# Performance work log

Hardware: AMD Instinct MI355X
Metric: run time of the kernel (lower is better)

## Reference

```python
import jax, jax.numpy as jnp
import numpy as np

N = 50000      # nodes
E = 400000     # edges
HID = 128      # hidden_size
L = 3          # num_att_layer
K = 9          # rbf_size
H = 4          # heads
C = HID // H   # out_channels per head (32)
G = 512        # graphs in batch
CUTOFF = 10.0


def _rbf(D):
    # ExponentialRBF: softplus(softplus_inverse(x)) == x, so centers/widths are the raw values
    centers = jnp.linspace(1.0, float(np.exp(-CUTOFF)), K)          # (K,)
    width = (0.5 / ((1.0 - np.exp(-CUTOFF)) / K)) ** 2              # scalar
    x = D / CUTOFF
    x3 = x ** 3
    x4 = x3 * x
    x5 = x4 * x
    cut = jnp.where(x < 1.0, 1.0 - 6.0 * x5 + 15.0 * x4 - 10.0 * x3, 0.0)
    return cut[:, None] * jnp.exp(-width * (jnp.exp(-D)[:, None] - centers) ** 2)  # (E,K)


def _ln(x, g, b):
    mu = jnp.mean(x, axis=-1, keepdims=True)
    var = jnp.var(x, axis=-1, keepdims=True)
    return (x - mu) / jnp.sqrt(var + 1e-5) * g + b


def _seg_softmax(logits, seg, n):
    # numerically stable softmax over edges grouped by target node
    m = jax.ops.segment_max(logits, seg, num_segments=n)
    e = jnp.exp(logits - m[seg])
    s = jax.ops.segment_sum(e, seg, num_segments=n)
    return e / s[seg]


def setup_inputs() -> dict:
    key = jax.random.key(0)
    ks = jax.random.split(key, 32)
    s = 1.0 / np.sqrt(HID)
    se = 1.0 / np.sqrt(K + 1)
    sb = 1.0 / np.sqrt(3 * HID)
    nrm = jax.random.normal
    inp = {
        "h": nrm(ks[0], (N, HID), jnp.float32),
        "pos": nrm(ks[1], (N, 3), jnp.float32) * 3.0,
        "edge_weight": jax.random.uniform(ks[2], (E,), jnp.float32),
        "Wq": nrm(ks[3], (L, HID, HID)) * s,   "bq": nrm(ks[4], (L, HID)) * 0.01,
        "Wk": nrm(ks[5], (L, HID, HID)) * s,   "bk": nrm(ks[6], (L, HID)) * 0.01,
        "Wv": nrm(ks[7], (L, HID, HID)) * s,   "bv": nrm(ks[8], (L, HID)) * 0.01,
        "We": nrm(ks[9], (L, K + 1, HID)) * se,
        "Wskip": nrm(ks[10], (L, HID, HID)) * s, "bskip": nrm(ks[11], (L, HID)) * 0.01,
        "Wbeta": nrm(ks[12], (L, 3 * HID, 1)) * sb,
        "Wffn1": nrm(ks[13], (L, HID, HID)) * s, "bffn1": nrm(ks[14], (L, HID)) * 0.01,
        "Wffn2": nrm(ks[15], (L, HID, HID)) * s, "bffn2": nrm(ks[16], (L, HID)) * 0.01,
        "Wffn3": nrm(ks[17], (L, HID, HID)) * s, "bffn3": nrm(ks[18], (L, HID)) * 0.01,
        "ln_g": jnp.ones((HID,), jnp.float32),
        "ln_b": jnp.zeros((HID,), jnp.float32),
        "Wo1": nrm(ks[19], (HID, HID)) * s, "bo1": nrm(ks[20], (HID,)) * 0.01,
        "Wo2": nrm(ks[21], (HID, 1)) * s,   "bo2": nrm(ks[22], (1,)) * 0.01,
        "edge_index": jax.random.randint(ks[23], (2, E), 0, N),
        "batch": jnp.sort(jax.random.randint(ks[24], (N,), 0, G)),
    }
    return inp


def reference(h, pos, edge_weight, Wq, bq, Wk, bk, Wv, bv, We, Wskip, bskip, Wbeta,
              Wffn1, bffn1, Wffn2, bffn2, Wffn3, bffn3, ln_g, ln_b, Wo1, bo1, Wo2, bo2,
              edge_index, batch):
    sp = jax.nn.softplus
    n = h.shape[0]
    src, dst = edge_index[0], edge_index[1]  # source j -> target i
    D = jnp.linalg.norm(pos[dst] - pos[src], axis=-1)              # (E,)
    efeat = jnp.concatenate([_rbf(D), edge_weight[:, None]], -1)   # (E, K+1)
    inv_sqrt_c = 1.0 / np.sqrt(C)

    for i in range(L):
        hn = _ln(h, ln_g, ln_b)
        q = (hn @ Wq[i] + bq[i]).reshape(n, H, C)
        k = (hn @ Wk[i] + bk[i]).reshape(n, H, C)
        v = (hn @ Wv[i] + bv[i]).reshape(n, H, C)
        ea = (efeat @ We[i]).reshape(-1, H, C)                     # (E,H,C)
        kj = k[src] + ea
        alpha = jnp.einsum('ehc,ehc->eh', q[dst], kj) * inv_sqrt_c  # (E,H)
        alpha = _seg_softmax(alpha, dst, n)
        # dropout p=0.5 is a no-op in eval mode
        msg = (v[src] + ea) * alpha[:, :, None]
        out = jax.ops.segment_sum(msg, dst, num_segments=n).reshape(n, H * C)
        x_r = hn @ Wskip[i] + bskip[i]
        beta = jax.nn.sigmoid(jnp.concatenate([out, x_r, out - x_r], -1) @ Wbeta[i])
        out = beta * x_r + (1.0 - beta) * out
        h = hn + sp(out)
        hn2 = _ln(h, ln_g, ln_b)
        f = sp(hn2 @ Wffn1[i] + bffn1[i])
        f = sp(f @ Wffn2[i] + bffn2[i])
        f = sp(f @ Wffn3[i] + bffn3[i])
        h = hn2 + f

    pooled = jax.ops.segment_sum(h, batch, num_segments=G)          # (G, HID)
    return sp(pooled @ Wo1 + bo1) @ Wo2 + bo2                       # (G, 1)
```

## Files before the change

kernel.cpp:

```cpp
#include <hip/hip_runtime.h>
#include <hip/hip_bf16.h>
#include <math.h>

#define HID 128
#define KRBF 9
#define NLAYER 3
#define IPAD 136

typedef __attribute__((ext_vector_type(8))) short bf16x8;
typedef __attribute__((ext_vector_type(4))) float f32x4;

__device__ __forceinline__ float sp_(float x){ return fmaxf(x,0.f) + log1pf(expf(-fabsf(x))); }
__device__ __forceinline__ float sigm_(float x){ return 1.f/(1.f+expf(-x)); }
__device__ __forceinline__ float b2f(short s){
  union{unsigned u; float f;} x; x.u = ((unsigned)(unsigned short)s)<<16; return x.f;
}
__device__ __forceinline__ short f2bs(float x){
  __hip_bfloat16 b = __float2bfloat16(x);
  return *reinterpret_cast<short*>(&b);
}
__device__ __forceinline__ float wsum64(float v){
  #pragma unroll
  for(int m=1;m<64;m<<=1) v += __shfl_xor(v,m,64);
  return v;
}
__device__ __forceinline__ float wsum16(float v){
  #pragma unroll
  for(int m=1;m<16;m<<=1) v += __shfl_xor(v,m,64);
  return v;
}
__device__ __forceinline__ float2 ldbf2(const __hip_bfloat16* p){
  __hip_bfloat162 b = *(const __hip_bfloat162*)p;
  return make_float2(__bfloat162float(b.x), __bfloat162float(b.y));
}
__device__ __forceinline__ int lb_(const int* __restrict__ a, int n, int key){
  int lo=0, hi=n;
  while(lo<hi){ int mid=(lo+hi)>>1; if(a[mid]<key) lo=mid+1; else hi=mid; }
  return lo;
}

__global__ void count_dst(const int* __restrict__ ei, int* __restrict__ counts, int E){
  int e = blockIdx.x*256+threadIdx.x;
  if(e<E) atomicAdd(&counts[ei[E+e]],1);
}
__global__ void scan1(const int* __restrict__ counts, int* __restrict__ tmp,
                      int* __restrict__ bsums, int N){
  __shared__ int lds[256];
  int t = threadIdx.x; int idx = blockIdx.x*256+t;
  int v = (idx<N)? counts[idx]:0;
  lds[t]=v; __syncthreads();
  for(int off=1;off<256;off<<=1){
    int x = (t>=off)? lds[t-off]:0;
    __syncthreads();
    lds[t]+=x; __syncthreads();
  }
  if(idx<N) tmp[idx]=lds[t];
  if(t==255) bsums[blockIdx.x]=lds[255];
}
__global__ void scan2(const int* __restrict__ bsums, int* __restrict__ boffs, int nb){
  __shared__ int lds[256];
  int t=threadIdx.x;
  int v = (t<nb)? bsums[t]:0;
  lds[t]=v; __syncthreads();
  for(int off=1;off<256;off<<=1){
    int x=(t>=off)?lds[t-off]:0;
    __syncthreads();
    lds[t]+=x; __syncthreads();
  }
  if(t<nb) boffs[t] = lds[t]-v;
}
__global__ void finalize_rs(const int* __restrict__ tmp, const int* __restrict__ boffs,
                            int* __restrict__ row_start, int N){
  int idx = blockIdx.x*256+threadIdx.x;
  if(idx<N) row_start[idx+1] = tmp[idx] + boffs[idx>>8];
  if(idx==0) row_start[0]=0;
}
__global__ void csr_scatter(const int* __restrict__ ei, const int* __restrict__ rowst,
                            int* __restrict__ counts2, int* __restrict__ csr, int E){
  int e = blockIdx.x*256+threadIdx.x;
  if(e>=E) return;
  int d = ei[E+e];
  int p = rowst[d] + atomicAdd(&counts2[d],1);
  csr[p] = e;
}
__global__ void sort_seg(const int* __restrict__ rowst, int* __restrict__ csr, int N){
  int n = blockIdx.x*256+threadIdx.x;
  if(n>=N) return;
  int lo=rowst[n], hi=rowst[n+1];
  for(int i=lo+1;i<hi;i++){
    int v=csr[i]; int j=i-1;
    while(j>=lo && csr[j]>v){ csr[j+1]=csr[j]; j--; }
    csr[j+1]=v;
  }
}
__global__ void edge_feat(const float* __restrict__ pos, const float* __restrict__ ew,
                          const int* __restrict__ ei, const int* __restrict__ csr,
                          float* __restrict__ efs, int* __restrict__ esrc, int E){
  int p = blockIdx.x*256 + threadIdx.x;
  if(p>=E) return;
  int e = csr[p];
  int s = ei[e], d = ei[E+e];
  float dx = pos[d*3+0]-pos[s*3+0];
  float dy = pos[d*3+1]-pos[s*3+1];
  float dz = pos[d*3+2]-pos[s*3+2];
  float D = sqrtf(dx*dx+dy*dy+dz*dz);
  float x = D*0.1f;
  float cut = 0.f;
  if(x < 1.f){ float x3=x*x*x, x4=x3*x, x5=x4*x; cut = 1.f - 6.f*x5 + 15.f*x4 - 10.f*x3; }
  float ed = expf(-D);
  const double e10 = 4.5399929762484854e-05;
  const float step  = (float)((e10 - 1.0)/8.0);
  const float width = (float)((4.5/(1.0-e10))*(4.5/(1.0-e10)));
  float r12[12];
  #pragma unroll
  for(int k=0;k<KRBF;k++){
    float c = 1.0f + k*step;
    float dd = ed - c;
    r12[k] = cut*expf(-width*dd*dd);
  }
  r12[9] = ew[e]; r12[10]=0.f; r12[11]=0.f;
  float* o = efs + (size_t)p*12;
  *(float4*)&o[0] = *(float4*)&r12[0];
  *(float4*)&o[4] = *(float4*)&r12[4];
  *(float4*)&o[8] = *(float4*)&r12[8];
  esrc[p] = s;
}

__global__ void pack_w(const float* __restrict__ Wq, const float* __restrict__ Wk,
                       const float* __restrict__ Wv, const float* __restrict__ Wsk,
                       const float* __restrict__ bq, const float* __restrict__ bk,
                       const float* __restrict__ bv, const float* __restrict__ bsk,
                       const float* __restrict__ We,
                       const float* __restrict__ W1, const float* __restrict__ W2,
                       const float* __restrict__ W3,
                       __hip_bfloat16* __restrict__ Wqkvs, float* __restrict__ bqkvs,
                       __hip_bfloat16* __restrict__ Wffn){
  int idx = blockIdx.x*256 + threadIdx.x;
  const int QT = NLAYER*5*16384;
  const int FT = NLAYER*3*16384;
  const int BT = NLAYER*640;
  if(idx < QT){
    int l = idx / (5*16384);
    int rem = idx - l*(5*16384);
    int cb = rem >> 14;
    int t = rem & 16383;
    int j = t&7; int lane = (t>>3)&63; int blk = t>>9;
    int kc = blk>>3, nj = blk&7, ql = lane>>4, il = lane&15;
    int k = kc*32 + ql*8 + j;
    int gcol = cb*128 + il*8 + nj;
    float v = 0.f;
    if(gcol < 512){
      const float* src = (gcol<128)?Wq:((gcol<256)?Wk:((gcol<384)?Wv:Wsk));
      v = src[(size_t)l*16384 + k*128 + (gcol&127)];
    } else if(gcol < 552){
      int jj = gcol-512; int h=jj/10; int r=jj-10*h;
      const float* wq = Wq + (size_t)l*16384 + k*128;
      const float* we = We + (size_t)l*1280 + r*128;
      float acc=0.f;
      #pragma unroll 8
      for(int c=32*h;c<32*h+32;c++) acc = fmaf(wq[c], we[c], acc);
      v = acc;
    }
    Wqkvs[idx] = __float2bfloat16(v);
  } else if(idx < QT+FT){
    int r0 = idx - QT;
    int l = r0 / (3*16384);
    int rem = r0 - l*(3*16384);
    int f = rem >> 14;
    int t = rem & 16383;
    int j = t&7; int lane = (t>>3)&63; int blk = t>>9;
    int kc = blk>>3, nj = blk&7, ql = lane>>4, il = lane&15;
    int k = kc*32 + ql*8 + j;
    int gcol = il*8 + nj;
    const float* src = (f==0)?W1:((f==1)?W2:W3);
    Wffn[r0] = __float2bfloat16(src[(size_t)l*16384 + k*128 + gcol]);
  } else if(idx < QT+FT+BT){
    int j = idx - QT - FT;
    int l = j/640; int col = j - l*640;
    float v = 0.f;
    if(col<512){
      const float* src = (col<128)?bq:((col<256)?bk:((col<384)?bv:bsk));
      v = src[l*128 + (col&127)];
    } else if(col<552){
      int jj=col-512; int h=jj/10; int r=jj-10*h;
      const float* bqp = bq + l*128;
      const float* we = We + (size_t)l*1280 + r*128;
      float acc=0.f;
      for(int c=32*h;c<32*h+32;c++) acc = fmaf(bqp[c], we[c], acc);
      v = acc;
    }
    bqkvs[j] = v;
  }
}

__global__ void ln_node(const float* __restrict__ h, const float* __restrict__ g,
                        const float* __restrict__ b, __hip_bfloat16* __restrict__ hn, int N){
  int n = blockIdx.x*4 + (threadIdx.x>>6);
  if(n>=N) return;
  int lane = threadIdx.x & 63;
  int c = 2*lane;
  float2 v = *(const float2*)&h[(size_t)n*HID + c];
  float s1 = wsum64(v.x+v.y);
  float s2 = wsum64(v.x*v.x+v.y*v.y);
  float mu = s1*(1.f/HID);
  float var = s2*(1.f/HID) - mu*mu;
  float rs = rsqrtf(var + 1e-5f);
  __hip_bfloat162 o;
  o.x = __float2bfloat16((v.x-mu)*rs*g[c]   + b[c]);
  o.y = __float2bfloat16((v.y-mu)*rs*g[c+1] + b[c+1]);
  *(__hip_bfloat162*)&hn[(size_t)n*HID + c] = o;
}

__global__ __launch_bounds__(256) void gemm_qkvs(
    const __hip_bfloat16* __restrict__ A, const __hip_bfloat16* __restrict__ Wt,
    const float* __restrict__ bias,
    __hip_bfloat16* __restrict__ qsO, __hip_bfloat16* __restrict__ kvO,
    float* __restrict__ qwO, int N){
  __shared__ __hip_bfloat16 WsF[16384];
  int row0 = blockIdx.y*128;
  int cb = blockIdx.x;
  int tid = threadIdx.x;
  {
    const __hip_bfloat16* Wp = Wt + (size_t)cb*16384;
    #pragma unroll
    for(int i=0;i<8;i++){
      int o = (tid + 256*i)*8;
      *(float4*)&WsF[o] = *(const float4*)&Wp[o];
    }
  }
  int lane = tid&63;
  int m0 = (tid>>6)*32;
  int ql = lane>>4, il = lane&15;
  bf16x8 af[2][4];
  #pragma unroll
  for(int mi=0;mi<2;mi++){
    int r = row0 + m0 + mi*16 + il;
    r = (r < N) ? r : (N-1);
    const __hip_bfloat16* ap = A + (size_t)r*128 + ql*8;
    #pragma unroll
    for(int kc=0;kc<4;kc++) af[mi][kc] = *(const bf16x8*)(ap + kc*32);
  }
  __syncthreads();
  f32x4 acc[2][8];
  #pragma unroll
  for(int mi=0;mi<2;mi++)
    #pragma unroll
    for(int nj=0;nj<8;nj++) acc[mi][nj] = (f32x4){0.f,0.f,0.f,0.f};
  #pragma unroll
  for(int kc=0;kc<4;kc++){
    #pragma unroll
    for(int nj=0;nj<8;nj++){
      bf16x8 bb = *(bf16x8*)&WsF[((kc*8+nj)*64 + lane)*8];
      #pragma unroll
      for(int mi=0;mi<2;mi++)
        acc[mi][nj] = __builtin_amdgcn_mfma_f32_16x16x32_bf16(af[mi][kc], bb, acc[mi][nj], 0,0,0);
    }
  }
  float bl8[8];
  {
    float4 b0 = *(const float4*)&bias[cb*128 + il*8];
    float4 b1 = *(const float4*)&bias[cb*128 + il*8 + 4];
    bl8[0]=b0.x; bl8[1]=b0.y; bl8[2]=b0.z; bl8[3]=b0.w;
    bl8[4]=b1.x; bl8[5]=b1.y; bl8[6]=b1.z; bl8[7]=b1.w;
  }
  #pragma unroll
  for(int mi=0;mi<2;mi++){
    #pragma unroll
    for(int r=0;r<4;r++){
      int rr = row0 + m0 + mi*16 + ql*4 + r;
      if(rr >= N) continue;
      if(cb < 4){
        bf16x8 o;
        #pragma unroll
        for(int nj=0;nj<8;nj++) o[nj] = f2bs(acc[mi][nj][r] + bl8[nj]);
        __hip_bfloat16* dst;
        if(cb==0)      dst = qsO + (size_t)rr*256 + il*8;
        else if(cb==1) dst = kvO + (size_t)rr*256 + il*8;
        else if(cb==2) dst = kvO + (size_t)rr*256 + 128 + il*8;
        else           dst = qsO + (size_t)rr*256 + 128 + il*8;
        *(bf16x8*)dst = o;
      } else if(il < 5){
        #pragma unroll
        for(int nj=0;nj<8;nj++){
          int g = il*8 + nj;
          int h = g/10, rb = g - 10*h;
          qwO[(size_t)rr*48 + h*12 + rb] = acc[mi][nj][r] + bl8[nj];
        }
      }
    }
  }
}

__global__ __launch_bounds__(256) void attn_fused6(
    const __hip_bfloat16* __restrict__ qs, const __hip_bfloat16* __restrict__ kvb,
    const float* __restrict__ qwb, const float* __restrict__ efs,
    const int* __restrict__ esrc, const float* __restrict__ WeL,
    const int* __restrict__ rowst, float* __restrict__ att, int N){
  int n = blockIdx.x*4 + (threadIdx.x>>6);
  if(n>=N) return;
  int lane = threadIdx.x & 63;
  int eg = lane>>4, sl = lane&15;
  int c8 = sl*8, hd = sl>>2;
  const __hip_bfloat16* rowq = qs + (size_t)n*256;
  float q8[8];
  {
    bf16x8 qv = *(const bf16x8*)&rowq[c8];
    #pragma unroll
    for(int j=0;j<8;j++) q8[j] = b2f(qv[j]);
  }
  const float* qwp = qwb + (size_t)n*48 + hd*12;
  float4 qa = *(const float4*)qwp;
  float4 qb = *(const float4*)(qwp+4);
  float2 qc = *(const float2*)(qwp+8);
  float QW[10] = {qa.x,qa.y,qa.z,qa.w,qb.x,qb.y,qb.z,qb.w,qc.x,qc.y};
  int lo = rowst[n], hi = rowst[n+1];
  float ssum = 0.f, a8[8], S[10];
  #pragma unroll
  for(int j=0;j<8;j++) a8[j]=0.f;
  #pragma unroll
  for(int r=0;r<10;r++) S[r]=0.f;
  for(int i=lo+eg; i<hi; i+=4){
    int s = esrc[i];
    const __hip_bfloat16* kr = kvb + (size_t)s*256;
    bf16x8 kc = *(const bf16x8*)&kr[c8];
    bf16x8 vc = *(const bf16x8*)&kr[128 + c8];
    const float* ef = efs + (size_t)i*12;
    float4 e0 = *(const float4*)&ef[0];
    float4 e1 = *(const float4*)&ef[4];
    float2 e2 = *(const float2*)&ef[8];
    float d = 0.f;
    #pragma unroll
    for(int j=0;j<8;j++) d = fmaf(q8[j], b2f(kc[j]), d);
    d += __shfl_xor(d,1,64); d += __shfl_xor(d,2,64);
    float lg = d;
    lg = fmaf(e0.x,QW[0],lg); lg = fmaf(e0.y,QW[1],lg);
    lg = fmaf(e0.z,QW[2],lg); lg = fmaf(e0.w,QW[3],lg);
    lg = fmaf(e1.x,QW[4],lg); lg = fmaf(e1.y,QW[5],lg);
    lg = fmaf(e1.z,QW[6],lg); lg = fmaf(e1.w,QW[7],lg);
    lg = fmaf(e2.x,QW[8],lg); lg = fmaf(e2.y,QW[9],lg);
    lg *= 0.17677669529663687f;
    lg = fminf(lg, 80.f);
    float w = __expf(lg);
    ssum += w;
    #pragma unroll
    for(int j=0;j<8;j++) a8[j] = fmaf(w, b2f(vc[j]), a8[j]);
    S[0]=fmaf(w,e0.x,S[0]); S[1]=fmaf(w,e0.y,S[1]); S[2]=fmaf(w,e0.z,S[2]);
    S[3]=fmaf(w,e0.w,S[3]); S[4]=fmaf(w,e1.x,S[4]); S[5]=fmaf(w,e1.y,S[5]);
    S[6]=fmaf(w,e1.z,S[6]); S[7]=fmaf(w,e1.w,S[7]); S[8]=fmaf(w,e2.x,S[8]);
    S[9]=fmaf(w,e2.y,S[9]);
  }
  float o8[8];
  #pragma unroll
  for(int j=0;j<8;j++) o8[j]=a8[j];
  #pragma unroll
  for(int r=0;r<10;r++){
    float s=S[r];
    float4 wa = *(const float4*)&WeL[r*128+c8];
    float4 wb = *(const float4*)&WeL[r*128+c8+4];
    o8[0]=fmaf(s,wa.x,o8[0]); o8[1]=fmaf(s,wa.y,o8[1]);
    o8[2]=fmaf(s,wa.z,o8[2]); o8[3]=fmaf(s,wa.w,o8[3]);
    o8[4]=fmaf(s,wb.x,o8[4]); o8[5]=fmaf(s,wb.y,o8[5]);
    o8[6]=fmaf(s,wb.z,o8[6]); o8[7]=fmaf(s,wb.w,o8[7]);
  }
  #pragma unroll
  for(int m=16;m<64;m<<=1){
    ssum += __shfl_xor(ssum,m,64);
    #pragma unroll
    for(int j=0;j<8;j++) o8[j] += __shfl_xor(o8[j],m,64);
  }
  if(eg==0){
    float inv = (hi>lo)? 1.f/ssum : 0.f;
    float4 v0 = make_float4(o8[0]*inv, o8[1]*inv, o8[2]*inv, o8[3]*inv);
    float4 v1 = make_float4(o8[4]*inv, o8[5]*inv, o8[6]*inv, o8[7]*inv);
    *(float4*)&att[(size_t)n*128 + c8]     = v0;
    *(float4*)&att[(size_t)n*128 + c8 + 4] = v1;
  }
}

__global__ void combine_ln(const float* __restrict__ att, const __hip_bfloat16* __restrict__ qs,
                           const __hip_bfloat16* __restrict__ hn, const float* __restrict__ Wb,
                           const float* __restrict__ g, const float* __restrict__ b,
                           __hip_bfloat16* __restrict__ hn2, int N){
  int n = blockIdx.x*4 + (threadIdx.x>>6);
  if(n>=N) return;
  int lane = threadIdx.x&63;
  int c = 2*lane;
  float2 o  = *(const float2*)&att[(size_t)n*HID+c];
  float2 xr = ldbf2(&qs[(size_t)n*256 + 128 + c]);
  float bl = o.x*Wb[c] + o.y*Wb[c+1]
           + xr.x*Wb[HID+c] + xr.y*Wb[HID+c+1]
           + (o.x-xr.x)*Wb[2*HID+c] + (o.y-xr.y)*Wb[2*HID+c+1];
  bl = wsum64(bl);
  float beta = sigm_(bl);
  float u0 = beta*xr.x + (1.f-beta)*o.x;
  float u1 = beta*xr.y + (1.f-beta)*o.y;
  float2 hnv = ldbf2(&hn[(size_t)n*HID+c]);
  float h0 = hnv.x + sp_(u0);
  float h1 = hnv.y + sp_(u1);
  float s1 = wsum64(h0+h1);
  float s2 = wsum64(h0*h0+h1*h1);
  float mu = s1*(1.f/HID);
  float var = s2*(1.f/HID)-mu*mu;
  float rs = rsqrtf(var+1e-5f);
  __hip_bfloat162 outv;
  outv.x = __float2bfloat16((h0-mu)*rs*g[c]+b[c]);
  outv.y = __float2bfloat16((h1-mu)*rs*g[c+1]+b[c+1]);
  *(__hip_bfloat162*)&hn2[(size_t)n*HID+c] = outv;
}

__global__ __launch_bounds__(256) void ffn_fused(
    const __hip_bfloat16* __restrict__ hn2, const __hip_bfloat16* __restrict__ Wf,
    const float* __restrict__ b1, const float* __restrict__ b2,
    const float* __restrict__ b3, const float* __restrict__ lng,
    const float* __restrict__ lnb, float* __restrict__ hout,
    __hip_bfloat16* __restrict__ hnout, int N){
  __shared__ __hip_bfloat16 WsF[16384];
  __shared__ __hip_bfloat16 inter[2][64][IPAD];
  int row0 = blockIdx.x*64;
  int tid = threadIdx.x, lane = tid&63, wv = tid>>6;
  int ql = lane>>4, il = lane&15;

  auto stage = [&](const __hip_bfloat16* Wp){
    #pragma unroll
    for(int i=0;i<8;i++){
      int o = (tid + 256*i)*8;
      *(float4*)&WsF[o] = *(const float4*)&Wp[o];
    }
  };
  auto loadbias = [&](const float* bp, float* bl8){
    float4 x0 = *(const float4*)&bp[il*8];
    float4 x1 = *(const float4*)&bp[il*8+4];
    bl8[0]=x0.x; bl8[1]=x0.y; bl8[2]=x0.z; bl8[3]=x0.w;
    bl8[4]=x1.x; bl8[5]=x1.y; bl8[6]=x1.z; bl8[7]=x1.w;
  };

  f32x4 acc[8];
  bf16x8 af[4];
  stage(Wf);
  {
    int r = row0 + wv*16 + il;
    r = (r<N)? r : (N-1);
    const __hip_bfloat16* ap = hn2 + (size_t)r*128 + ql*8;
    #pragma unroll
    for(int kc=0;kc<4;kc++) af[kc] = *(const bf16x8*)(ap + kc*32);
  }
  __syncthreads();
  #pragma unroll
  for(int nj=0;nj<8;nj++) acc[nj] = (f32x4){0.f,0.f,0.f,0.f};
  #pragma unroll
  for(int kc=0;kc<4;kc++)
    #pragma unroll
    for(int nj=0;nj<8;nj++){
      bf16x8 bb = *(bf16x8*)&WsF[((kc*8+nj)*64 + lane)*8];
      acc[nj] = __builtin_amdgcn_mfma_f32_16x16x32_bf16(af[kc], bb, acc[nj], 0,0,0);
    }
  {
    float bl8[8]; loadbias(b1, bl8);
    #pragma unroll
    for(int r=0;r<4;r++){
      int lr = wv*16 + ql*4 + r;
      bf16x8 o;
      #pragma unroll
      for(int nj=0;nj<8;nj++) o[nj] = f2bs(sp_(acc[nj][r] + bl8[nj]));
      *(bf16x8*)&inter[0][lr][il*8] = o;
    }
  }
  __syncthreads();
  stage(Wf + 16384);
  #pragma unroll
  for(int kc=0;kc<4;kc++) af[kc] = *(bf16x8*)&inter[0][wv*16+il][ql*8 + kc*32];
  __syncthreads();
  #pragma unroll
  for(int nj=0;nj<8;nj++) acc[nj] = (f32x4){0.f,0.f,0.f,0.f};
  #pragma unroll
  for(int kc=0;kc<4;kc++)
    #pragma unroll
    for(int nj=0;nj<8;nj++){
      bf16x8 bb = *(bf16x8*)&WsF[((kc*8+nj)*64 + lane)*8];
      acc[nj] = __builtin_amdgcn_mfma_f32_16x16x32_bf16(af[kc], bb, acc[nj], 0,0,0);
    }
  {
    float bl8[8]; loadbias(b2, bl8);
    #pragma unroll
    for(int r=0;r<4;r++){
      int lr = wv*16 + ql*4 + r;
      bf16x8 o;
      #pragma unroll
      for(int nj=0;nj<8;nj++) o[nj] = f2bs(sp_(acc[nj][r] + bl8[nj]));
      *(bf16x8*)&inter[1][lr][il*8] = o;
    }
  }
  __syncthreads();
  stage(Wf + 2*16384);
  #pragma unroll
  for(int kc=0;kc<4;kc++) af[kc] = *(bf16x8*)&inter[1][wv*16+il][ql*8 + kc*32];
  __syncthreads();
  #pragma unroll
  for(int nj=0;nj<8;nj++) acc[nj] = (f32x4){0.f,0.f,0.f,0.f};
  #pragma unroll
  for(int kc=0;kc<4;kc++)
    #pragma unroll
    for(int nj=0;nj<8;nj++){
      bf16x8 bb = *(bf16x8*)&WsF[((kc*8+nj)*64 + lane)*8];
      acc[nj] = __builtin_amdgcn_mfma_f32_16x16x32_bf16(af[kc], bb, acc[nj], 0,0,0);
    }
  {
    float bl8[8]; loadbias(b3, bl8);
    float lg8[8], lb8[8];
    loadbias(lng, lg8); loadbias(lnb, lb8);
    #pragma unroll
    for(int r=0;r<4;r++){
      int rr = row0 + wv*16 + ql*4 + r;
      if(rr >= N) continue;
      bf16x8 rv = *(const bf16x8*)&hn2[(size_t)rr*128 + il*8];
      float t8[8], s1=0.f, s2=0.f;
      #pragma unroll
      for(int nj=0;nj<8;nj++){
        float x = sp_(acc[nj][r] + bl8[nj]) + b2f(rv[nj]);
        t8[nj]=x; s1+=x; s2+=x*x;
      }
      s1 = wsum16(s1); s2 = wsum16(s2);
      float mu = s1*(1.f/128.f);
      float var = s2*(1.f/128.f) - mu*mu;
      float rsg = rsqrtf(var + 1e-5f);
      *(float4*)&hout[(size_t)rr*128 + il*8]     = make_float4(t8[0],t8[1],t8[2],t8[3]);
      *(float4*)&hout[(size_t)rr*128 + il*8 + 4] = make_float4(t8[4],t8[5],t8[6],t8[7]);
      bf16x8 o;
      #pragma unroll
      for(int nj=0;nj<8;nj++) o[nj] = f2bs((t8[nj]-mu)*rsg*lg8[nj] + lb8[nj]);
      *(bf16x8*)&hnout[(size_t)rr*128 + il*8] = o;
    }
  }
}

__global__ void pool_head(const float* __restrict__ h, const int* __restrict__ batch,
                          const float* __restrict__ Wo1, const float* __restrict__ bo1,
                          const float* __restrict__ Wo2, const float* __restrict__ bo2,
                          float* __restrict__ out, int N){
  int gid = blockIdx.x;
  int t = threadIdx.x;
  int lo = lb_(batch, N, gid), hi = lb_(batch, N, gid+1);
  __shared__ float pl[128];
  __shared__ float red[128];
  float s = 0.f;
  for(int i=lo;i<hi;i++) s += h[(size_t)i*HID + t];
  pl[t] = s;
  __syncthreads();
  float acc = bo1[t];
  for(int c=0;c<128;c++) acc = fmaf(pl[c], Wo1[c*HID+t], acc);
  red[t] = sp_(acc)*Wo2[t];
  __syncthreads();
  for(int off=64;off>0;off>>=1){
    if(t<off) red[t]+=red[t+off];
    __syncthreads();
  }
  if(t==0) out[gid] = red[0] + bo2[0];
}

extern "C" void kernel_launch(void* const* d_in, const int* in_sizes, int n_in,
                              void* d_out, int out_size, void* d_ws, size_t ws_size,
                              hipStream_t stream){
  const float* h_in = (const float*)d_in[0];
  const float* pos  = (const float*)d_in[1];
  const float* ew   = (const float*)d_in[2];
  const float* Wq = (const float*)d_in[3];  const float* bq = (const float*)d_in[4];
  const float* Wk = (const float*)d_in[5];  const float* bk = (const float*)d_in[6];
  const float* Wv = (const float*)d_in[7];  const float* bv = (const float*)d_in[8];
  const float* We = (const float*)d_in[9];
  const float* Wsk= (const float*)d_in[10]; const float* bsk=(const float*)d_in[11];
  const float* Wbeta=(const float*)d_in[12];
  const float* W1=(const float*)d_in[13]; const float* b1=(const float*)d_in[14];
  const float* W2=(const float*)d_in[15]; const float* b2=(const float*)d_in[16];
  const float* W3=(const float*)d_in[17]; const float* b3=(const float*)d_in[18];
  const float* lng=(const float*)d_in[19]; const float* lnb=(const float*)d_in[20];
  const float* Wo1=(const float*)d_in[21]; const float* bo1=(const float*)d_in[22];
  const float* Wo2=(const float*)d_in[23]; const float* bo2=(const float*)d_in[24];
  const int* ei    = (const int*)d_in[25];
  const int* batch = (const int*)d_in[26];
  int N = in_sizes[0]/HID;
  int E = in_sizes[2];
  int G = out_size;
  float* out = (float*)d_out;

  char* ws = (char*)d_ws;
  size_t off=0;
  auto alloc=[&](size_t bytes)->char*{
    char* p = ws + off;
    off = (off + bytes + 255) & ~(size_t)255;
    return p;
  };
  float* efs   =(float*)alloc((size_t)E*12*4);
  int* esrc    =(int*)  alloc((size_t)E*4);
  int* csr     =(int*)  alloc((size_t)E*4);
  int* counts  =(int*)  alloc((size_t)N*4);
  int* counts2 =(int*)  alloc((size_t)N*4);
  int* rowst   =(int*)  alloc((size_t)(N+1)*4);
  int* tmp     =(int*)  alloc((size_t)N*4);
  int* bsums   =(int*)  alloc(256*4);
  int* boffs   =(int*)  alloc(256*4);
  __hip_bfloat16* hn   =(__hip_bfloat16*)alloc((size_t)N*HID*2);
  __hip_bfloat16* hn2  =(__hip_bfloat16*)alloc((size_t)N*HID*2);
  __hip_bfloat16* qsb  =(__hip_bfloat16*)alloc((size_t)N*256*2);
  __hip_bfloat16* kvb  =(__hip_bfloat16*)alloc((size_t)N*256*2);
  float* qwb   =(float*)alloc((size_t)N*48*4);
  float* att   =(float*)alloc((size_t)N*HID*4);
  float* hcur  =(float*)alloc((size_t)N*HID*4);
  __hip_bfloat16* Wqkvs_t =(__hip_bfloat16*)alloc((size_t)NLAYER*5*16384*2);
  __hip_bfloat16* Wffn_t  =(__hip_bfloat16*)alloc((size_t)NLAYER*3*16384*2);
  float* bqkvs =(float*)alloc((size_t)NLAYER*640*4);
  size_t ws_used = off;

  int ebl = (E+255)/256;
  int nb  = (N+255)/256;
  int nwb = (N+3)/4;
  int nrb128 = (N+127)/128;
  int nrb64  = (N+63)/64;
  dim3 gqkvs(5, nrb128);

  hipMemsetAsync(ws, 0, (ws_used <= ws_size ? ws_used : ws_size), stream);

  count_dst<<<ebl,256,0,stream>>>(ei,counts,E);
  scan1<<<nb,256,0,stream>>>(counts,tmp,bsums,N);
  scan2<<<1,256,0,stream>>>(bsums,boffs,nb);
  finalize_rs<<<nb,256,0,stream>>>(tmp,boffs,rowst,N);
  csr_scatter<<<ebl,256,0,stream>>>(ei,rowst,counts2,csr,E);
  sort_seg<<<nb,256,0,stream>>>(rowst,csr,N);
  edge_feat<<<ebl,256,0,stream>>>(pos,ew,ei,csr,efs,esrc,E);
  {
    int tot = NLAYER*5*16384 + NLAYER*3*16384 + NLAYER*640;
    pack_w<<<(tot+255)/256,256,0,stream>>>(Wq,Wk,Wv,Wsk,bq,bk,bv,bsk,We,W1,W2,W3,
                                           Wqkvs_t,bqkvs,Wffn_t);
  }

  ln_node<<<nwb,256,0,stream>>>(h_in,lng,lnb,hn,N);
  for(int l=0;l<NLAYER;l++){
    const float* We_l = We + (size_t)l*(KRBF+1)*HID;
    const float* Wb_l = Wbeta + (size_t)l*3*HID;
    const float* b1_l = b1 + (size_t)l*HID;
    const float* b2_l = b2 + (size_t)l*HID;
    const float* b3_l = b3 + (size_t)l*HID;

    gemm_qkvs<<<gqkvs,256,0,stream>>>(hn, Wqkvs_t + (size_t)l*5*16384,
                                      bqkvs + l*640, qsb, kvb, qwb, N);
    attn_fused6<<<nwb,256,0,stream>>>(qsb,kvb,qwb,efs,esrc,We_l,rowst,att,N);
    combine_ln<<<nwb,256,0,stream>>>(att,qsb,hn,Wb_l,lng,lnb,hn2,N);
    ffn_fused<<<nrb64,256,0,stream>>>(hn2, Wffn_t + (size_t)l*3*16384,
                                      b1_l,b2_l,b3_l,lng,lnb,hcur,hn,N);
  }
  pool_head<<<G,128,0,stream>>>(hcur,batch,Wo1,bo1,Wo2,bo2,out,N);
}
```

Baseline: 883.1 us.

## Switch activations to fp32 and emulate fp32 GEMMs with split-bf16 MFMAs

Replaces bf16 activation storage with fp32 throughout (hn, q/k/v/skip, FFN intermediates). The GEMMs now split each fp32 operand into hi/mid/lo bf16 parts and issue six MFMAs per tile, with weights read straight from global memory instead of being staged in LDS. Softplus and sigmoid now use fast __expf/__logf intrinsics. The aim is accuracy close to fp32, paid for with twice the gather bandwidth in attention, six times the MFMA work, and extra weight traffic.

```diff
diff --git a/kernel.cpp b/kernel.cpp
--- a/kernel.cpp
+++ b/kernel.cpp
@@ -5,13 +5,15 @@
 #define HID 128
 #define KRBF 9
 #define NLAYER 3
-#define IPAD 136
+#define IPADF 132
 
 typedef __attribute__((ext_vector_type(8))) short bf16x8;
 typedef __attribute__((ext_vector_type(4))) float f32x4;
 
-__device__ __forceinline__ float sp_(float x){ return fmaxf(x,0.f) + log1pf(expf(-fabsf(x))); }
-__device__ __forceinline__ float sigm_(float x){ return 1.f/(1.f+expf(-x)); }
+__device__ __forceinline__ float sp_(float x){
+  return fmaxf(x,0.f) + __logf(1.f + __expf(-fabsf(x)));
+}
+__device__ __forceinline__ float sigm_(float x){ return 1.f/(1.f+__expf(-x)); }
 __device__ __forceinline__ float b2f(short s){
   union{unsigned u; float f;} x; x.u = ((unsigned)(unsigned short)s)<<16; return x.f;
 }
@@ -19,6 +21,16 @@
   __hip_bfloat16 b = __float2bfloat16(x);
   return *reinterpret_cast<short*>(&b);
 }
+__device__ __forceinline__ void split3_8(const float* a, bf16x8& hi, bf16x8& mi, bf16x8& lo){
+  #pragma unroll
+  for(int j=0;j<8;j++){
+    float x = a[j];
+    short h = f2bs(x); hi[j]=h;
+    float r1 = x - b2f(h);
+    short m = f2bs(r1); mi[j]=m;
+    lo[j] = f2bs(r1 - b2f(m));
+  }
+}
 __device__ __forceinline__ float wsum64(float v){
   #pragma unroll
   for(int m=1;m<64;m<<=1) v += __shfl_xor(v,m,64);
@@ -28,10 +40,6 @@
   #pragma unroll
   for(int m=1;m<16;m<<=1) v += __shfl_xor(v,m,64);
   return v;
-}
-__device__ __forceinline__ float2 ldbf2(const __hip_bfloat16* p){
-  __hip_bfloat162 b = *(const __hip_bfloat162*)p;
-  return make_float2(__bfloat162float(b.x), __bfloat162float(b.y));
 }
 __device__ __forceinline__ int lb_(const int* __restrict__ a, int n, int key){
   int lo=0, hi=n;
@@ -161,7 +169,13 @@
       for(int c=32*h;c<32*h+32;c++) acc = fmaf(wq[c], we[c], acc);
       v = acc;
     }
-    Wqkvs[idx] = __float2bfloat16(v);
+    short hi = f2bs(v);
+    float r1 = v - b2f(hi);
+    short mi = f2bs(r1);
+    short lo = f2bs(r1 - b2f(mi));
+    Wqkvs[idx]        = *reinterpret_cast<__hip_bfloat16*>(&hi);
+    Wqkvs[QT + idx]   = *reinterpret_cast<__hip_bfloat16*>(&mi);
+    Wqkvs[2*QT + idx] = *reinterpret_cast<__hip_bfloat16*>(&lo);
   } else if(idx < QT+FT){
     int r0 = idx - QT;
     int l = r0 / (3*16384);
@@ -173,7 +187,14 @@
     int k = kc*32 + ql*8 + j;
     int gcol = il*8 + nj;
     const float* src = (f==0)?W1:((f==1)?W2:W3);
-    Wffn[r0] = __float2bfloat16(src[(size_t)l*16384 + k*128 + gcol]);
+    float v = src[(size_t)l*16384 + k*128 + gcol];
+    short hi = f2bs(v);
+    float r1 = v - b2f(hi);
+    short mi = f2bs(r1);
+    short lo = f2bs(r1 - b2f(mi));
+    Wffn[r0]        = *reinterpret_cast<__hip_bfloat16*>(&hi);
+    Wffn[FT + r0]   = *reinterpret_cast<__hip_bfloat16*>(&mi);
+    Wffn[2*FT + r0] = *reinterpret_cast<__hip_bfloat16*>(&lo);
   } else if(idx < QT+FT+BT){
     int j = idx - QT - FT;
     int l = j/640; int col = j - l*640;
@@ -194,7 +215,7 @@
 }
 
 __global__ void ln_node(const float* __restrict__ h, const float* __restrict__ g,
-                        const float* __restrict__ b, __hip_bfloat16* __restrict__ hn, int N){
+                        const float* __restrict__ b, float* __restrict__ hn, int N){
   int n = blockIdx.x*4 + (threadIdx.x>>6);
   if(n>=N) return;
   int lane = threadIdx.x & 63;
@@ -205,55 +226,68 @@
   float mu = s1*(1.f/HID);
   float var = s2*(1.f/HID) - mu*mu;
   float rs = rsqrtf(var + 1e-5f);
-  __hip_bfloat162 o;
-  o.x = __float2bfloat16((v.x-mu)*rs*g[c]   + b[c]);
-  o.y = __float2bfloat16((v.y-mu)*rs*g[c+1] + b[c+1]);
-  *(__hip_bfloat162*)&hn[(size_t)n*HID + c] = o;
-}
+  float2 o;
+  o.x = (v.x-mu)*rs*g[c]   + b[c];
+  o.y = (v.y-mu)*rs*g[c+1] + b[c+1];
+  *(float2*)&hn[(size_t)n*HID + c] = o;
+}
+
+#define MFMA6(ACC, AH, AM, AL, BH, BM, BL)                                    \
+  ACC = __builtin_amdgcn_mfma_f32_16x16x32_bf16(AH, BH, ACC, 0,0,0);          \
+  ACC = __builtin_amdgcn_mfma_f32_16x16x32_bf16(AM, BH, ACC, 0,0,0);          \
+  ACC = __builtin_amdgcn_mfma_f32_16x16x32_bf16(AH, BM, ACC, 0,0,0);          \
+  ACC = __builtin_amdgcn_mfma_f32_16x16x32_bf16(AL, BH, ACC, 0,0,0);          \
+  ACC = __builtin_amdgcn_mfma_f32_16x16x32_bf16(AM, BM, ACC, 0,0,0);          \
+  ACC = __builtin_amdgcn_mfma_f32_16x16x32_bf16(AH, BL, ACC, 0,0,0);
 
 __global__ __launch_bounds__(256) void gemm_qkvs(
-    const __hip_bfloat16* __restrict__ A, const __hip_bfloat16* __restrict__ Wt,
+    const float* __restrict__ A, const __hip_bfloat16* __restrict__ Whi,
+    const __hip_bfloat16* __restrict__ Wmi, const __hip_bfloat16* __restrict__ Wlo,
     const float* __restrict__ bias,
-    __hip_bfloat16* __restrict__ qsO, __hip_bfloat16* __restrict__ kvO,
+    float* __restrict__ qsO, float* __restrict__ kvO,
     float* __restrict__ qwO, int N){
-  __shared__ __hip_bfloat16 WsF[16384];
   int row0 = blockIdx.y*128;
   int cb = blockIdx.x;
   int tid = threadIdx.x;
-  {
-    const __hip_bfloat16* Wp = Wt + (size_t)cb*16384;
-    #pragma unroll
-    for(int i=0;i<8;i++){
-      int o = (tid + 256*i)*8;
-      *(float4*)&WsF[o] = *(const float4*)&Wp[o];
-    }
-  }
   int lane = tid&63;
   int m0 = (tid>>6)*32;
   int ql = lane>>4, il = lane&15;
-  bf16x8 af[2][4];
-  #pragma unroll
-  for(int mi=0;mi<2;mi++){
-    int r = row0 + m0 + mi*16 + il;
+  const __hip_bfloat16* Wh = Whi + (size_t)cb*16384;
+  const __hip_bfloat16* Wm = Wmi + (size_t)cb*16384;
+  const __hip_bfloat16* Wl = Wlo + (size_t)cb*16384;
+  bf16x8 ah[2][4], am[2][4], al[2][4];
+  #pragma unroll
+  for(int mi2=0;mi2<2;mi2++){
+    int r = row0 + m0 + mi2*16 + il;
     r = (r < N) ? r : (N-1);
-    const __hip_bfloat16* ap = A + (size_t)r*128 + ql*8;
-    #pragma unroll
-    for(int kc=0;kc<4;kc++) af[mi][kc] = *(const bf16x8*)(ap + kc*32);
-  }
-  __syncthreads();
+    const float* ap = A + (size_t)r*128 + ql*8;
+    #pragma unroll
+    for(int kc=0;kc<4;kc++){
+      float a8[8];
+      float4 a0 = *(const float4*)(ap + kc*32);
+      float4 a1 = *(const float4*)(ap + kc*32 + 4);
+      a8[0]=a0.x;a8[1]=a0.y;a8[2]=a0.z;a8[3]=a0.w;
+      a8[4]=a1.x;a8[5]=a1.y;a8[6]=a1.z;a8[7]=a1.w;
+      split3_8(a8, ah[mi2][kc], am[mi2][kc], al[mi2][kc]);
+    }
+  }
   f32x4 acc[2][8];
   #pragma unroll
-  for(int mi=0;mi<2;mi++)
-    #pragma unroll
-    for(int nj=0;nj<8;nj++) acc[mi][nj] = (f32x4){0.f,0.f,0.f,0.f};
+  for(int mi2=0;mi2<2;mi2++)
+    #pragma unroll
+    for(int nj=0;nj<8;nj++) acc[mi2][nj] = (f32x4){0.f,0.f,0.f,0.f};
   #pragma unroll
   for(int kc=0;kc<4;kc++){
     #pragma unroll
     for(int nj=0;nj<8;nj++){
-      bf16x8 bb = *(bf16x8*)&WsF[((kc*8+nj)*64 + lane)*8];
+      size_t bo = (size_t)((kc*8+nj)*64 + lane)*8;
+      bf16x8 bh = *(const bf16x8*)&Wh[bo];
+      bf16x8 bm = *(const bf16x8*)&Wm[bo];
+      bf16x8 bl = *(const bf16x8*)&Wl[bo];
       #pragma unroll
-      for(int mi=0;mi<2;mi++)
-        acc[mi][nj] = __builtin_amdgcn_mfma_f32_16x16x32_bf16(af[mi][kc], bb, acc[mi][nj], 0,0,0);
+      for(int mi2=0;mi2<2;mi2++){
+        MFMA6(acc[mi2][nj], ah[mi2][kc], am[mi2][kc], al[mi2][kc], bh, bm, bl)
+      }
     }
   }
   float bl8[8];
@@ -264,35 +298,36 @@
     bl8[4]=b1.x; bl8[5]=b1.y; bl8[6]=b1.z; bl8[7]=b1.w;
   }
   #pragma unroll
-  for(int mi=0;mi<2;mi++){
+  for(int mi2=0;mi2<2;mi2++){
     #pragma unroll
     for(int r=0;r<4;r++){
-      int rr = row0 + m0 + mi*16 + ql*4 + r;
+      int rr = row0 + m0 + mi2*16 + ql*4 + r;
       if(rr >= N) continue;
       if(cb < 4){
-        bf16x8 o;
+        float o8[8];
         #pragma unroll
-        for(int nj=0;nj<8;nj++) o[nj] = f2bs(acc[mi][nj][r] + bl8[nj]);
-        __hip_bfloat16* dst;
+        for(int nj=0;nj<8;nj++) o8[nj] = acc[mi2][nj][r] + bl8[nj];
+        float* dst;
         if(cb==0)      dst = qsO + (size_t)rr*256 + il*8;
         else if(cb==1) dst = kvO + (size_t)rr*256 + il*8;
         else if(cb==2) dst = kvO + (size_t)rr*256 + 128 + il*8;
         else           dst = qsO + (size_t)rr*256 + 128 + il*8;
-        *(bf16x8*)dst = o;
+        *(float4*)dst     = make_float4(o8[0],o8[1],o8[2],o8[3]);
+        *(float4*)(dst+4) = make_float4(o8[4],o8[5],o8[6],o8[7]);
       } else if(il < 5){
         #pragma unroll
         for(int nj=0;nj<8;nj++){
           int g = il*8 + nj;
           int h = g/10, rb = g - 10*h;
-          qwO[(size_t)rr*48 + h*12 + rb] = acc[mi][nj][r] + bl8[nj];
+          qwO[(size_t)rr*48 + h*12 + rb] = acc[mi2][nj][r] + bl8[nj];
         }
       }
     }
   }
 }
 
-__global__ __launch_bounds__(256) void attn_fused6(
-    const __hip_bfloat16* __restrict__ qs, const __hip_bfloat16* __restrict__ kvb,
+__global__ __launch_bounds__(256) void attn_fused7(
+    const float* __restrict__ qs, const float* __restrict__ kvb,
     const float* __restrict__ qwb, const float* __restrict__ efs,
     const int* __restrict__ esrc, const float* __restrict__ WeL,
     const int* __restrict__ rowst, float* __restrict__ att, int N){
@@ -301,12 +336,13 @@
   int lane = threadIdx.x & 63;
   int eg = lane>>4, sl = lane&15;
   int c8 = sl*8, hd = sl>>2;
-  const __hip_bfloat16* rowq = qs + (size_t)n*256;
+  const float* rowq = qs + (size_t)n*256;
   float q8[8];
   {
-    bf16x8 qv = *(const bf16x8*)&rowq[c8];
-    #pragma unroll
-    for(int j=0;j<8;j++) q8[j] = b2f(qv[j]);
+    float4 q0 = *(const float4*)&rowq[c8];
+    float4 q1 = *(const float4*)&rowq[c8+4];
+    q8[0]=q0.x;q8[1]=q0.y;q8[2]=q0.z;q8[3]=q0.w;
+    q8[4]=q1.x;q8[5]=q1.y;q8[6]=q1.z;q8[7]=q1.w;
   }
   const float* qwp = qwb + (size_t)n*48 + hd*12;
   float4 qa = *(const float4*)qwp;
@@ -321,16 +357,17 @@
   for(int r=0;r<10;r++) S[r]=0.f;
   for(int i=lo+eg; i<hi; i+=4){
     int s = esrc[i];
-    const __hip_bfloat16* kr = kvb + (size_t)s*256;
-    bf16x8 kc = *(const bf16x8*)&kr[c8];
-    bf16x8 vc = *(const bf16x8*)&kr[128 + c8];
+    const float* kr = kvb + (size_t)s*256;
+    float4 k0 = *(const float4*)&kr[c8];
+    float4 k1 = *(const float4*)&kr[c8+4];
+    float4 v0 = *(const float4*)&kr[128+c8];
+    float4 v1 = *(const float4*)&kr[128+c8+4];
     const float* ef = efs + (size_t)i*12;
     float4 e0 = *(const float4*)&ef[0];
     float4 e1 = *(const float4*)&ef[4];
     float2 e2 = *(const float2*)&ef[8];
-    float d = 0.f;
-    #pragma unroll
-    for(int j=0;j<8;j++) d = fmaf(q8[j], b2f(kc[j]), d);
+    float d = q8[0]*k0.x + q8[1]*k0.y + q8[2]*k0.z + q8[3]*k0.w
+            + q8[4]*k1.x + q8[5]*k1.y + q8[6]*k1.z + q8[7]*k1.w;
     d += __shfl_xor(d,1,64); d += __shfl_xor(d,2,64);
     float lg = d;
     lg = fmaf(e0.x,QW[0],lg); lg = fmaf(e0.y,QW[1],lg);
@@ -342,8 +379,10 @@
     lg = fminf(lg, 80.f);
     float w = __expf(lg);
     ssum += w;
-    #pragma unroll
-    for(int j=0;j<8;j++) a8[j] = fmaf(w, b2f(vc[j]), a8[j]);
+    a8[0]=fmaf(w,v0.x,a8[0]); a8[1]=fmaf(w,v0.y,a8[1]);
+    a8[2]=fmaf(w,v0.z,a8[2]); a8[3]=fmaf(w,v0.w,a8[3]);
+    a8[4]=fmaf(w,v1.x,a8[4]); a8[5]=fmaf(w,v1.y,a8[5]);
+    a8[6]=fmaf(w,v1.z,a8[6]); a8[7]=fmaf(w,v1.w,a8[7]);
     S[0]=fmaf(w,e0.x,S[0]); S[1]=fmaf(w,e0.y,S[1]); S[2]=fmaf(w,e0.z,S[2]);
     S[3]=fmaf(w,e0.w,S[3]); S[4]=fmaf(w,e1.x,S[4]); S[5]=fmaf(w,e1.y,S[5]);
     S[6]=fmaf(w,e1.z,S[6]); S[7]=fmaf(w,e1.w,S[7]); S[8]=fmaf(w,e2.x,S[8]);
@@ -377,16 +416,16 @@
   }
 }
 
-__global__ void combine_ln(const float* __restrict__ att, const __hip_bfloat16* __restrict__ qs,
-                           const __hip_bfloat16* __restrict__ hn, const float* __restrict__ Wb,
+__global__ void combine_ln(const float* __restrict__ att, float* __restrict__ qs,
+                           const float* __restrict__ hn, const float* __restrict__ Wb,
                            const float* __restrict__ g, const float* __restrict__ b,
-                           __hip_bfloat16* __restrict__ hn2, int N){
+                           int N){
   int n = blockIdx.x*4 + (threadIdx.x>>6);
   if(n>=N) return;
   int lane = threadIdx.x&63;
   int c = 2*lane;
   float2 o  = *(const float2*)&att[(size_t)n*HID+c];
-  float2 xr = ldbf2(&qs[(size_t)n*256 + 128 + c]);
+  float2 xr = *(const float2*)&qs[(size_t)n*256 + 128 + c];
   float bl = o.x*Wb[c] + o.y*Wb[c+1]
            + xr.x*Wb[HID+c] + xr.y*Wb[HID+c+1]
            + (o.x-xr.x)*Wb[2*HID+c] + (o.y-xr.y)*Wb[2*HID+c+1];
@@ -394,7 +433,7 @@
   float beta = sigm_(bl);
   float u0 = beta*xr.x + (1.f-beta)*o.x;
   float u1 = beta*xr.y + (1.f-beta)*o.y;
-  float2 hnv = ldbf2(&hn[(size_t)n*HID+c]);
+  float2 hnv = *(const float2*)&hn[(size_t)n*HID+c];
   float h0 = hnv.x + sp_(u0);
   float h1 = hnv.y + sp_(u1);
   float s1 = wsum64(h0+h1);
@@ -402,108 +441,111 @@
   float mu = s1*(1.f/HID);
   float var = s2*(1.f/HID)-mu*mu;
   float rs = rsqrtf(var+1e-5f);
-  __hip_bfloat162 outv;
-  outv.x = __float2bfloat16((h0-mu)*rs*g[c]+b[c]);
-  outv.y = __float2bfloat16((h1-mu)*rs*g[c+1]+b[c+1]);
-  *(__hip_bfloat162*)&hn2[(size_t)n*HID+c] = outv;
+  float2 outv;
+  outv.x = (h0-mu)*rs*g[c]+b[c];
+  outv.y = (h1-mu)*rs*g[c+1]+b[c+1];
+  *(float2*)&qs[(size_t)n*256 + c] = outv;
 }
 
 __global__ __launch_bounds__(256) void ffn_fused(
-    const __hip_bfloat16* __restrict__ hn2, const __hip_bfloat16* __restrict__ Wf,
+    const float* __restrict__ hn2,
+    const __hip_bfloat16* __restrict__ Wfhi, const __hip_bfloat16* __restrict__ Wfmi,
+    const __hip_bfloat16* __restrict__ Wflo,
     const float* __restrict__ b1, const float* __restrict__ b2,
     const float* __restrict__ b3, const float* __restrict__ lng,
     const float* __restrict__ lnb, float* __restrict__ hout,
-    __hip_bfloat16* __restrict__ hnout, int N){
-  __shared__ __hip_bfloat16 WsF[16384];
-  __shared__ __hip_bfloat16 inter[2][64][IPAD];
+    float* __restrict__ hnout, int N){
+  __shared__ float inter[2][64][IPADF];
   int row0 = blockIdx.x*64;
   int tid = threadIdx.x, lane = tid&63, wv = tid>>6;
   int ql = lane>>4, il = lane&15;
 
-  auto stage = [&](const __hip_bfloat16* Wp){
-    #pragma unroll
-    for(int i=0;i<8;i++){
-      int o = (tid + 256*i)*8;
-      *(float4*)&WsF[o] = *(const float4*)&Wp[o];
-    }
-  };
   auto loadbias = [&](const float* bp, float* bl8){
     float4 x0 = *(const float4*)&bp[il*8];
     float4 x1 = *(const float4*)&bp[il*8+4];
     bl8[0]=x0.x; bl8[1]=x0.y; bl8[2]=x0.z; bl8[3]=x0.w;
     bl8[4]=x1.x; bl8[5]=x1.y; bl8[6]=x1.z; bl8[7]=x1.w;
   };
+  auto gemm_stage = [&](const __hip_bfloat16* Wh, const __hip_bfloat16* Wm,
+                        const __hip_bfloat16* Wl,
+                        bf16x8* ah, bf16x8* am, bf16x8* al, f32x4* acc){
+    #pragma unroll
+    for(int nj=0;nj<8;nj++) acc[nj] = (f32x4){0.f,0.f,0.f,0.f};
+    #pragma unroll
+    for(int kc=0;kc<4;kc++)
+      #pragma unroll
+      for(int nj=0;nj<8;nj++){
+        size_t bo = (size_t)((kc*8+nj)*64 + lane)*8;
+        bf16x8 bh = *(const bf16x8*)&Wh[bo];
+        bf16x8 bm = *(const bf16x8*)&Wm[bo];
+        bf16x8 bl = *(const bf16x8*)&Wl[bo];
+        MFMA6(acc[nj], ah[kc], am[kc], al[kc], bh, bm, bl)
+      }
+  };
 
   f32x4 acc[8];
-  bf16x8 af[4];
-  stage(Wf);
+  bf16x8 ah[4], am[4], al[4];
   {
     int r = row0 + wv*16 + il;
     r = (r<N)? r : (N-1);
-    const __hip_bfloat16* ap = hn2 + (size_t)r*128 + ql*8;
-    #pragma unroll
-    for(int kc=0;kc<4;kc++) af[kc] = *(const bf16x8*)(ap + kc*32);
-  }
-  __syncthreads();
-  #pragma unroll
-  for(int nj=0;nj<8;nj++) acc[nj] = (f32x4){0.f,0.f,0.f,0.f};
-  #pragma unroll
-  for(int kc=0;kc<4;kc++)
-    #pragma unroll
-    for(int nj=0;nj<8;nj++){
-      bf16x8 bb = *(bf16x8*)&WsF[((kc*8+nj)*64 + lane)*8];
-      acc[nj] = __builtin_amdgcn_mfma_f32_16x16x32_bf16(af[kc], bb, acc[nj], 0,0,0);
-    }
+    const float* ap = hn2 + (size_t)r*256 + ql*8;
+    #pragma unroll
+    for(int kc=0;kc<4;kc++){
+      float a8[8];
+      float4 a0 = *(const float4*)(ap + kc*32);
+      float4 a1 = *(const float4*)(ap + kc*32 + 4);
+      a8[0]=a0.x;a8[1]=a0.y;a8[2]=a0.z;a8[3]=a0.w;
+      a8[4]=a1.x;a8[5]=a1.y;a8[6]=a1.z;a8[7]=a1.w;
+      split3_8(a8, ah[kc], am[kc], al[kc]);
+    }
+  }
+  gemm_stage(Wfhi, Wfmi, Wflo, ah, am, al, acc);
   {
     float bl8[8]; loadbias(b1, bl8);
     #pragma unroll
     for(int r=0;r<4;r++){
       int lr = wv*16 + ql*4 + r;
-      bf16x8 o;
+      float o8[8];
       #pragma unroll
-      for(int nj=0;nj<8;nj++) o[nj] = f2bs(sp_(acc[nj][r] + bl8[nj]));
-      *(bf16x8*)&inter[0][lr][il*8] = o;
+      for(int nj=0;nj<8;nj++) o8[nj] = sp_(acc[nj][r] + bl8[nj]);
+      *(float4*)&inter[0][lr][il*8]   = make_float4(o8[0],o8[1],o8[2],o8[3]);
+      *(float4*)&inter[0][lr][il*8+4] = make_float4(o8[4],o8[5],o8[6],o8[7]);
     }
   }
   __syncthreads();
-  stage(Wf + 16384);
-  #pragma unroll
-  for(int kc=0;kc<4;kc++) af[kc] = *(bf16x8*)&inter[0][wv*16+il][ql*8 + kc*32];
-  __syncthreads();
-  #pragma unroll
-  for(int nj=0;nj<8;nj++) acc[nj] = (f32x4){0.f,0.f,0.f,0.f};
-  #pragma unroll
-  for(int kc=0;kc<4;kc++)
-    #pragma unroll
-    for(int nj=0;nj<8;nj++){
-      bf16x8 bb = *(bf16x8*)&WsF[((kc*8+nj)*64 + lane)*8];
-      acc[nj] = __builtin_amdgcn_mfma_f32_16x16x32_bf16(af[kc], bb, acc[nj], 0,0,0);
-    }
+  #pragma unroll
+  for(int kc=0;kc<4;kc++){
+    float a8[8];
+    float4 a0 = *(float4*)&inter[0][wv*16+il][ql*8 + kc*32];
+    float4 a1 = *(float4*)&inter[0][wv*16+il][ql*8 + kc*32 + 4];
+    a8[0]=a0.x;a8[1]=a0.y;a8[2]=a0.z;a8[3]=a0.w;
+    a8[4]=a1.x;a8[5]=a1.y;a8[6]=a1.z;a8[7]=a1.w;
+    split3_8(a8, ah[kc], am[kc], al[kc]);
+  }
+  gemm_stage(Wfhi + 16384, Wfmi + 16384, Wflo + 16384, ah, am, al, acc);
   {
     float bl8[8]; loadbias(b2, bl8);
     #pragma unroll
     for(int r=0;r<4;r++){
       int lr = wv*16 + ql*4 + r;
-      bf16x8 o;
+      float o8[8];
       #pragma unroll
-      for(int nj=0;nj<8;nj++) o[nj] = f2bs(sp_(acc[nj][r] + bl8[nj]));
-      *(bf16x8*)&inter[1][lr][il*8] = o;
+      for(int nj=0;nj<8;nj++) o8[nj] = sp_(acc[nj][r] + bl8[nj]);
+      *(float4*)&inter[1][lr][il*8]   = make_float4(o8[0],o8[1],o8[2],o8[3]);
+      *(float4*)&inter[1][lr][il*8+4] = make_float4(o8[4],o8[5],o8[6],o8[7]);
     }
   }
   __syncthreads();
-  stage(Wf + 2*16384);
-  #pragma unroll
-  for(int kc=0;kc<4;kc++) af[kc] = *(bf16x8*)&inter[1][wv*16+il][ql*8 + kc*32];
-  __syncthreads();
-  #pragma unroll
-  for(int nj=0;nj<8;nj++) acc[nj] = (f32x4){0.f,0.f,0.f,0.f};
-  #pragma unroll
-  for(int kc=0;kc<4;kc++)
-    #pragma unroll
-    for(int nj=0;nj<8;nj++){
-      bf16x8 bb = *(bf16x8*)&WsF[((kc*8+nj)*64 + lane)*8];
-      acc[nj] = __builtin_amdgcn_mfma_f32_16x16x32_bf16(af[kc], bb, acc[nj], 0,0,0);
-    }
+  #pragma unroll
+  for(int kc=0;kc<4;kc++){
+    float a8[8];
+    float4 a0 = *(float4*)&inter[1][wv*16+il][ql*8 + kc*32];
+    float4 a1 = *(float4*)&inter[1][wv*16+il][ql*8 + kc*32 + 4];
+    a8[0]=a0.x;a8[1]=a0.y;a8[2]=a0.z;a8[3]=a0.w;
+    a8[4]=a1.x;a8[5]=a1.y;a8[6]=a1.z;a8[7]=a1.w;
+    split3_8(a8, ah[kc], am[kc], al[kc]);
+  }
+  gemm_stage(Wfhi + 2*16384, Wfmi + 2*16384, Wflo + 2*16384, ah, am, al, acc);
   {
     float bl8[8]; loadbias(b3, bl8);
     float lg8[8], lb8[8];
@@ -512,11 +554,18 @@
     for(int r=0;r<4;r++){
       int rr = row0 + wv*16 + ql*4 + r;
       if(rr >= N) continue;
-      bf16x8 rv = *(const bf16x8*)&hn2[(size_t)rr*128 + il*8];
+      float rv8[8];
+      {
+        const float* rp = hn2 + (size_t)rr*256 + il*8;
+        float4 r0 = *(const float4*)rp;
+        float4 r1 = *(const float4*)(rp+4);
+        rv8[0]=r0.x;rv8[1]=r0.y;rv8[2]=r0.z;rv8[3]=r0.w;
+        rv8[4]=r1.x;rv8[5]=r1.y;rv8[6]=r1.z;rv8[7]=r1.w;
+      }
       float t8[8], s1=0.f, s2=0.f;
       #pragma unroll
       for(int nj=0;nj<8;nj++){
-        float x = sp_(acc[nj][r] + bl8[nj]) + b2f(rv[nj]);
+        float x = sp_(acc[nj][r] + bl8[nj]) + rv8[nj];
         t8[nj]=x; s1+=x; s2+=x*x;
       }
       s1 = wsum16(s1); s2 = wsum16(s2);
@@ -525,10 +574,11 @@
       float rsg = rsqrtf(var + 1e-5f);
       *(float4*)&hout[(size_t)rr*128 + il*8]     = make_float4(t8[0],t8[1],t8[2],t8[3]);
       *(float4*)&hout[(size_t)rr*128 + il*8 + 4] = make_float4(t8[4],t8[5],t8[6],t8[7]);
-      bf16x8 o;
+      float o8[8];
       #pragma unroll
-      for(int nj=0;nj<8;nj++) o[nj] = f2bs((t8[nj]-mu)*rsg*lg8[nj] + lb8[nj]);
-      *(bf16x8*)&hnout[(size_t)rr*128 + il*8] = o;
+      for(int nj=0;nj<8;nj++) o8[nj] = (t8[nj]-mu)*rsg*lg8[nj] + lb8[nj];
+      *(float4*)&hnout[(size_t)rr*128 + il*8]     = make_float4(o8[0],o8[1],o8[2],o8[3]);
+      *(float4*)&hnout[(size_t)rr*128 + il*8 + 4] = make_float4(o8[4],o8[5],o8[6],o8[7]);
     }
   }
 }
@@ -598,18 +648,19 @@
   int* tmp     =(int*)  alloc((size_t)N*4);
   int* bsums   =(int*)  alloc(256*4);
   int* boffs   =(int*)  alloc(256*4);
-  __hip_bfloat16* hn   =(__hip_bfloat16*)alloc((size_t)N*HID*2);
-  __hip_bfloat16* hn2  =(__hip_bfloat16*)alloc((size_t)N*HID*2);
-  __hip_bfloat16* qsb  =(__hip_bfloat16*)alloc((size_t)N*256*2);
-  __hip_bfloat16* kvb  =(__hip_bfloat16*)alloc((size_t)N*256*2);
+  float* hnf   =(float*)alloc((size_t)N*HID*4);
+  float* qsb   =(float*)alloc((size_t)N*256*4);
+  float* kvb   =(float*)alloc((size_t)N*256*4);
   float* qwb   =(float*)alloc((size_t)N*48*4);
   float* att   =(float*)alloc((size_t)N*HID*4);
   float* hcur  =(float*)alloc((size_t)N*HID*4);
-  __hip_bfloat16* Wqkvs_t =(__hip_bfloat16*)alloc((size_t)NLAYER*5*16384*2);
-  __hip_bfloat16* Wffn_t  =(__hip_bfloat16*)alloc((size_t)NLAYER*3*16384*2);
+  __hip_bfloat16* Wqkvs_t =(__hip_bfloat16*)alloc((size_t)3*NLAYER*5*16384*2);
+  __hip_bfloat16* Wffn_t  =(__hip_bfloat16*)alloc((size_t)3*NLAYER*3*16384*2);
   float* bqkvs =(float*)alloc((size_t)NLAYER*640*4);
   size_t ws_used = off;
 
+  const int QT = NLAYER*5*16384;
+  const int FT = NLAYER*3*16384;
   int ebl = (E+255)/256;
   int nb  = (N+255)/256;
   int nwb = (N+3)/4;
@@ -627,25 +678,31 @@
   sort_seg<<<nb,256,0,stream>>>(rowst,csr,N);
   edge_feat<<<ebl,256,0,stream>>>(pos,ew,ei,csr,efs,esrc,E);
   {
-    int tot = NLAYER*5*16384 + NLAYER*3*16384 + NLAYER*640;
+    int tot = QT + FT + NLAYER*640;
     pack_w<<<(tot+255)/256,256,0,stream>>>(Wq,Wk,Wv,Wsk,bq,bk,bv,bsk,We,W1,W2,W3,
                                            Wqkvs_t,bqkvs,Wffn_t);
   }
 
-  ln_node<<<nwb,256,0,stream>>>(h_in,lng,lnb,hn,N);
+  ln_node<<<nwb,256,0,stream>>>(h_in,lng,lnb,hnf,N);
   for(int l=0;l<NLAYER;l++){
     const float* We_l = We + (size_t)l*(KRBF+1)*HID;
     const float* Wb_l = Wbeta + (size_t)l*3*HID;
     const float* b1_l = b1 + (size_t)l*HID;
     const float* b2_l = b2 + (size_t)l*HID;
     const float* b3_l = b3 + (size_t)l*HID;
-
-    gemm_qkvs<<<gqkvs,256,0,stream>>>(hn, Wqkvs_t + (size_t)l*5*16384,
-                                      bqkvs + l*640, qsb, kvb, qwb, N);
-    attn_fused6<<<nwb,256,0,stream>>>(qsb,kvb,qwb,efs,esrc,We_l,rowst,att,N);
-    combine_ln<<<nwb,256,0,stream>>>(att,qsb,hn,Wb_l,lng,lnb,hn2,N);
-    ffn_fused<<<nrb64,256,0,stream>>>(hn2, Wffn_t + (size_t)l*3*16384,
-                                      b1_l,b2_l,b3_l,lng,lnb,hcur,hn,N);
+    const __hip_bfloat16* Wq_hi = Wqkvs_t + (size_t)l*5*16384;
+    const __hip_bfloat16* Wq_mi = Wqkvs_t + QT + (size_t)l*5*16384;
+    const __hip_bfloat16* Wq_lo = Wqkvs_t + 2*(size_t)QT + (size_t)l*5*16384;
+    const __hip_bfloat16* Wf_hi = Wffn_t + (size_t)l*3*16384;
+    const __hip_bfloat16* Wf_mi = Wffn_t + FT + (size_t)l*3*16384;
+    const __hip_bfloat16* Wf_lo = Wffn_t + 2*(size_t)FT + (size_t)l*3*16384;
+
+    gemm_qkvs<<<gqkvs,256,0,stream>>>(hnf, Wq_hi, Wq_mi, Wq_lo, bqkvs + l*640,
+                                      qsb, kvb, qwb, N);
+    attn_fused7<<<nwb,256,0,stream>>>(qsb,kvb,qwb,efs,esrc,We_l,rowst,att,N);
+    combine_ln<<<nwb,256,0,stream>>>(att,qsb,hnf,Wb_l,lng,lnb,N);
+    ffn_fused<<<nrb64,256,0,stream>>>(qsb, Wf_hi, Wf_mi, Wf_lo,
+                                      b1_l,b2_l,b3_l,lng,lnb,hcur,hnf,N);
   }
   pool_head<<<G,128,0,stream>>>(hcur,batch,Wo1,bo1,Wo2,bo2,out,N);
 }
```

After: 988.2 us (median of 2 runs). +11.9%, slower.
